# Performance work log

Measured on AMD Instinct MI355X. Metric: run time of the kernel, lower is better.

Reference implementation:

```python
import jax, jax.numpy as jnp
import numpy as np

B, H, D, HD = 16384, 8, 256, 128  # batch, heads, dim, hidden_dim


def setup_inputs() -> dict:
    key = jax.random.key(0)
    ks = jax.random.split(key, 8)
    return {
        "x": jax.random.normal(ks[0], (B, D), dtype=jnp.float32),
        "h": jax.random.normal(ks[1], (B, H, HD), dtype=jnp.float32),
        "sigmoid_w": jax.random.normal(ks[2], (H, HD + D, 2), dtype=jnp.float32),
        "sigmoid_b": jax.random.normal(ks[3], (H, 2), dtype=jnp.float32),
        "tanh_w": jax.random.normal(ks[4], (H, HD + D, HD), dtype=jnp.float32),
        "tanh_b": jax.random.normal(ks[5], (H, HD), dtype=jnp.float32),
        "out_w": jax.random.normal(ks[6], (H, HD, D), dtype=jnp.float32),
        "out_b": jax.random.normal(ks[7], (H, D), dtype=jnp.float32),
    }


def reference(x, h, sigmoid_w, sigmoid_b, tanh_w, tanh_b, out_w, out_b):
    # x: [B, D] -> broadcast across heads: [B, H, D]
    x_ = jnp.broadcast_to(x[:, None, :], (x.shape[0], h.shape[1], x.shape[1]))
    # gate input: [B, H, hidden+dim]
    sig_in = jnp.concatenate([h, x_], axis=2)
    sigmoids = jax.nn.sigmoid(jnp.einsum('bhm,hmn->bhn', sig_in, sigmoid_w) + sigmoid_b)
    # reset-gated hidden concat with x: [B, H, hidden+dim]
    tanh_in = jnp.concatenate([sigmoids[:, :, :1] * h, x_], axis=2)
    cand = jnp.tanh(jnp.einsum('bhm,hmn->bhn', tanh_in, tanh_w) + tanh_b)
    proportion = sigmoids[:, :, 1:]
    new_h = (1 - proportion) * h + proportion * cand
    output = jnp.einsum('bhm,hmn->bhn', new_h, out_w) + out_b
    return (output, new_h)
```

## Files before the change

### kernel.cpp

```cpp
#include <hip/hip_runtime.h>
#include <math.h>

typedef short bf16x8 __attribute__((ext_vector_type(8)));
typedef short bf16x4 __attribute__((ext_vector_type(4)));
typedef float floatx4 __attribute__((ext_vector_type(4)));
typedef float floatx2 __attribute__((ext_vector_type(2)));
typedef float floatx16 __attribute__((ext_vector_type(16)));

#define NB   16384
#define H8   8
#define ND   256
#define NHD  128
#define NK   384

__device__ __forceinline__ unsigned short f2bf(float f) {
  unsigned int u = __float_as_uint(f);
  u += 0x7FFFu + ((u >> 16) & 1u);
  return (unsigned short)(u >> 16);
}
__device__ __forceinline__ float bf2f(unsigned short s) {
  return __uint_as_float(((unsigned int)s) << 16);
}
__device__ __forceinline__ float fast_sigmoid(float z) {
  z = fminf(fmaxf(z, -60.f), 60.f);
  return __builtin_amdgcn_rcpf(1.f + __expf(-z));
}
__device__ __forceinline__ float fast_tanh(float s) {
  s = fminf(fmaxf(s, -9.f), 9.f);
  float e = __expf(2.f * s);
  return (e - 1.f) * __builtin_amdgcn_rcpf(e + 1.f);
}

#define WTP (H8 * 24 * 4 * 512)
#define WOP (H8 * 8 * 8 * 512)
#define XFP (NB * ND)
#define NGATE (NB * H8)
#define WS_NEED3 ((size_t)(WTP + WOP + XFP) * 2 + (size_t)2 * NGATE * 4)

__global__ void prep3c(const float* __restrict__ tanh_w,
                       const float* __restrict__ sig_w,
                       const float* __restrict__ sig_b,
                       const float* __restrict__ out_w,
                       const float* __restrict__ x,
                       const float* __restrict__ h,
                       short* __restrict__ wtp_hi,
                       short* __restrict__ wop,
                       short* __restrict__ xfh,
                       float* __restrict__ gW, float* __restrict__ pW) {
  __shared__ float smem[14480];
  const int t = threadIdx.x;
  const int b = blockIdx.x;
  if (b < 192) {
    float* tile = smem;
    int head = b / 24, ks = b % 24;
    const float* slab = tanh_w + ((size_t)head * NK + ks * 16) * NHD;
#pragma unroll
    for (int it = 0; it < 2; ++it) {
      int i = it * 256 + t;
      floatx4 v = reinterpret_cast<const floatx4*>(slab)[i];
      int r = i >> 5, c4 = i & 31;
      *reinterpret_cast<floatx4*>(&tile[r * 132 + c4 * 4]) = v;
    }
    __syncthreads();
    int ct = t >> 6, l = t & 63;
    bf16x8 hi8;
#pragma unroll
    for (int j = 0; j < 8; ++j) {
      float w = tile[((l >> 5) * 8 + j) * 132 + ct * 32 + (l & 31)];
      hi8[j] = (short)f2bf(w);
    }
    size_t dst = ((((size_t)head * 24 + ks) * 4 + ct) * 64 + l) * 8;
    *reinterpret_cast<bf16x8*>(wtp_hi + dst) = hi8;
  } else if (b < 256) {
    float* tile = smem;
    int head = (b - 192) / 8, ks = (b - 192) % 8;
    const float* slab = out_w + ((size_t)head * NHD + ks * 16) * ND;
#pragma unroll
    for (int it = 0; it < 4; ++it) {
      int i = it * 256 + t;
      floatx4 v = reinterpret_cast<const floatx4*>(slab)[i];
      int r = i >> 6, c4 = i & 63;
      *reinterpret_cast<floatx4*>(&tile[r * 260 + c4 * 4]) = v;
    }
    __syncthreads();
#pragma unroll
    for (int u = 0; u < 2; ++u) {
      int idx = u * 256 + t;
      int ct = idx >> 6, l = idx & 63;
      bf16x8 o8;
#pragma unroll
      for (int j = 0; j < 8; ++j) {
        float w = tile[((l >> 5) * 8 + j) * 260 + ct * 32 + (l & 31)];
        o8[j] = (short)f2bf(w);
      }
      size_t dst = ((((size_t)head * 8 + ks) * 8 + ct) * 64 + l) * 8;
      *reinterpret_cast<bf16x8*>(wop + dst) = o8;
    }
  } else if (b < 2304) {
    int i = (b - 256) * 256 + t;
    int bb = i >> 5, c0 = (i & 31) * 8;
    const float* xp = x + (size_t)bb * ND + c0;
    floatx4 v0 = *reinterpret_cast<const floatx4*>(xp);
    floatx4 v1 = *reinterpret_cast<const floatx4*>(xp + 4);
    bf16x8 h8;
#pragma unroll
    for (int j = 0; j < 4; ++j) {
      h8[j] = (short)f2bf(v0[j]);
      h8[4 + j] = (short)f2bf(v1[j]);
    }
    int dst = ((bb >> 5) * 16 + (c0 >> 4)) * 512 +
              (((c0 >> 3) & 1) * 32 + (bb & 31)) * 8;
    *reinterpret_cast<bf16x8*>(xfh + dst) = h8;
  } else {
    float* xs = smem;
    float* ws = smem + 8320;
    int gb = b - 2304;
    long rowb = (long)gb * 32;
#pragma unroll
    for (int it = 0; it < 8; ++it) {
      int idx = it * 256 + t;
      int r = idx >> 6, c4 = idx & 63;
      floatx4 v = *reinterpret_cast<const floatx4*>(x + (rowb + r) * ND + c4 * 4);
      *reinterpret_cast<floatx4*>(&xs[r * 260 + c4 * 4]) = v;
    }
#pragma unroll
    for (int it = 0; it < 12; ++it) {
      int idx = it * 256 + t;
      floatx2 v = *reinterpret_cast<const floatx2*>(sig_w + (size_t)idx * 2);
      int head = idx / 384;
      int rem = idx * 2 - head * 768;
      *reinterpret_cast<floatx2*>(&ws[head * 770 + rem]) = v;
    }
    __syncthreads();
    int bl = t >> 3, head = t & 7;
    const float* hrow = h + (rowb * 8 + t) * 128;
    const float* wh = &ws[head * 770];
    float a0 = 0.f, a1 = 0.f;
#pragma unroll 8
    for (int k4 = 0; k4 < 32; ++k4) {
      floatx4 hv = *reinterpret_cast<const floatx4*>(hrow + k4 * 4);
#pragma unroll
      for (int j = 0; j < 4; ++j) {
        floatx2 w2 = *reinterpret_cast<const floatx2*>(&wh[(k4 * 4 + j) * 2]);
        a0 += hv[j] * w2[0];
        a1 += hv[j] * w2[1];
      }
    }
    const float* xrow = &xs[bl * 260];
#pragma unroll 8
    for (int k4 = 0; k4 < 64; ++k4) {
      floatx4 xv = *reinterpret_cast<const floatx4*>(xrow + k4 * 4);
#pragma unroll
      for (int j = 0; j < 4; ++j) {
        floatx2 w2 = *reinterpret_cast<const floatx2*>(&wh[(128 + k4 * 4 + j) * 2]);
        a0 += xv[j] * w2[0];
        a1 += xv[j] * w2[1];
      }
    }
    long gi = rowb * 8 + t;
    gW[gi] = fast_sigmoid(a0 + sig_b[head * 2 + 0]);
    pW[gi] = fast_sigmoid(a1 + sig_b[head * 2 + 1]);
  }
}

__global__ __launch_bounds__(256, 4) void gru3(
    const float* __restrict__ h,
    const float* __restrict__ tanh_b, const float* __restrict__ out_b,
    const short* __restrict__ wtp_hi, const short* __restrict__ wop,
    const short* __restrict__ xfh,
    const float* __restrict__ gW, const float* __restrict__ pW,
    float* __restrict__ out, float* __restrict__ out_nh) {
  __shared__ __align__(16) short AhH[16 * 512];
  __shared__ __align__(16) short AhL[16 * 512];
  __shared__ float pbuf[64];

  const int t = threadIdx.x;
  const int lane = t & 63;
  const int cq = t >> 6;
  const int l31 = lane & 31;
  const int lh = lane >> 5;
  const int head = (int)(blockIdx.x >> 8);
  const int rb = (int)(blockIdx.x & 255);
  const long rowbase = (long)rb * 64;

  if (t < 64) pbuf[t] = pW[(rowbase + t) * H8 + head];

#pragma unroll
  for (int it = 0; it < 4; ++it) {
    int gi = it * 256 + t;
    int row = gi >> 4, kc = gi & 15;
    float g = gW[(rowbase + row) * H8 + head];
    const float* hp = h + ((rowbase + row) * H8 + head) * NHD + kc * 8;
    floatx4 v0 = *reinterpret_cast<const floatx4*>(hp);
    floatx4 v1 = *reinterpret_cast<const floatx4*>(hp + 4);
    bf16x8 hi8, lo8;
#pragma unroll
    for (int j = 0; j < 4; ++j) {
      float s0 = g * v0[j];
      unsigned short hb = f2bf(s0);
      hi8[j] = (short)hb; lo8[j] = (short)f2bf(s0 - bf2f(hb));
      float s1 = g * v1[j];
      unsigned short hb2 = f2bf(s1);
      hi8[4 + j] = (short)hb2; lo8[4 + j] = (short)f2bf(s1 - bf2f(hb2));
    }
    int rg = row >> 5, row32 = row & 31;
    int chunk = (rg * 8 + (kc >> 1)) * 64 + (kc & 1) * 32 + row32;
    *reinterpret_cast<bf16x8*>(&AhH[chunk * 8]) = hi8;
    *reinterpret_cast<bf16x8*>(&AhL[chunk * 8]) = lo8;
  }
  __syncthreads();

  const short* __restrict__ xh0 = xfh + ((size_t)(rb * 2 + 0) * 16 * 512) + lane * 8;
  const short* __restrict__ xh1 = xfh + ((size_t)(rb * 2 + 1) * 16 * 512) + lane * 8;
  const short* __restrict__ bh_p = wtp_hi + (((size_t)head * 24 * 4 + cq) * 512) + lane * 8;

  floatx16 acc0, acc1;
#pragma unroll
  for (int z = 0; z < 16; ++z) { acc0[z] = 0.f; acc1[z] = 0.f; }

  bf16x8 bhA = *reinterpret_cast<const bf16x8*>(bh_p);
  bf16x8 bhB = *reinterpret_cast<const bf16x8*>(bh_p + 2048);
#pragma unroll
  for (int ks = 0; ks < 8; ++ks) {
    bf16x8 bh = bhA; bhA = bhB;
    bhB = *reinterpret_cast<const bf16x8*>(bh_p + (ks + 2) * 2048);
    bf16x8 a0h = *reinterpret_cast<const bf16x8*>(&AhH[(ks * 64 + lane) * 8]);
    bf16x8 a0l = *reinterpret_cast<const bf16x8*>(&AhL[(ks * 64 + lane) * 8]);
    bf16x8 a1h = *reinterpret_cast<const bf16x8*>(&AhH[((8 + ks) * 64 + lane) * 8]);
    bf16x8 a1l = *reinterpret_cast<const bf16x8*>(&AhL[((8 + ks) * 64 + lane) * 8]);
    acc0 = __builtin_amdgcn_mfma_f32_32x32x16_bf16(a0h, bh, acc0, 0, 0, 0);
    acc0 = __builtin_amdgcn_mfma_f32_32x32x16_bf16(a0l, bh, acc0, 0, 0, 0);
    acc1 = __builtin_amdgcn_mfma_f32_32x32x16_bf16(a1h, bh, acc1, 0, 0, 0);
    acc1 = __builtin_amdgcn_mfma_f32_32x32x16_bf16(a1l, bh, acc1, 0, 0, 0);
  }
  {
    bf16x8 x0A = *reinterpret_cast<const bf16x8*>(xh0);
    bf16x8 x1A = *reinterpret_cast<const bf16x8*>(xh1);
    bf16x8 x0B = *reinterpret_cast<const bf16x8*>(xh0 + 512);
    bf16x8 x1B = *reinterpret_cast<const bf16x8*>(xh1 + 512);
#pragma unroll
    for (int xk = 0; xk < 16; ++xk) {
      const int ks = 8 + xk;
      bf16x8 bh = bhA; bhA = bhB;
      if (ks + 2 < 24) bhB = *reinterpret_cast<const bf16x8*>(bh_p + (ks + 2) * 2048);
      bf16x8 x0 = x0A, x1 = x1A;
      x0A = x0B; x1A = x1B;
      if (xk + 2 < 16) {
        x0B = *reinterpret_cast<const bf16x8*>(xh0 + (xk + 2) * 512);
        x1B = *reinterpret_cast<const bf16x8*>(xh1 + (xk + 2) * 512);
      }
      acc0 = __builtin_amdgcn_mfma_f32_32x32x16_bf16(x0, bh, acc0, 0, 0, 0);
      acc1 = __builtin_amdgcn_mfma_f32_32x32x16_bf16(x1, bh, acc1, 0, 0, 0);
    }
  }
  __syncthreads();

  const int col = cq * 32 + l31;
  const float tb = tanh_b[head * NHD + col];
  const float* __restrict__ hcol = h + (rowbase * H8 + head) * NHD + col;
#define EPI(RG, ACC)                                                          \
  {                                                                           \
    _Pragma("unroll")                                                         \
    for (int reg = 0; reg < 16; ++reg) {                                      \
      int crow = (reg & 3) + 8 * (reg >> 2) + 4 * lh;                         \
      int row = RG * 32 + crow;                                               \
      float p = pbuf[row];                                                    \
      float cand = fast_tanh(ACC[reg] + tb);                                  \
      float hv = hcol[(size_t)row * (H8 * NHD)];                              \
      float nh = hv + p * (cand - hv);                                        \
      int el = ((RG * 8 + (col >> 4)) * 64 + ((l31 >> 3) & 1) * 32 + crow) * 8 + (col & 7); \
      out_nh[((rowbase + row) * H8 + head) * NHD + col] = nh;                 \
      AhH[el] = (short)f2bf(nh);                                              \
    }                                                                         \
  }
  EPI(0, acc0)
  EPI(1, acc1)
#undef EPI
  __syncthreads();

  const short* __restrict__ wo_p = wop + (((size_t)head * 64 + cq * 2) * 512) + lane * 8;
  const float ob0 = out_b[head * ND + cq * 64 + l31];
  const float ob1 = out_b[head * ND + cq * 64 + 32 + l31];
#define OUTP(RG)                                                              \
  {                                                                           \
    floatx16 a3a, a3b;                                                        \
    _Pragma("unroll")                                                         \
    for (int z = 0; z < 16; ++z) { a3a[z] = 0.f; a3b[z] = 0.f; }              \
    bf16x8 w0n = *reinterpret_cast<const bf16x8*>(wo_p);                      \
    bf16x8 w1n = *reinterpret_cast<const bf16x8*>(wo_p + 512);                \
    _Pragma("unroll")                                                         \
    for (int ks = 0; ks < 8; ++ks) {                                          \
      bf16x8 w0 = w0n, w1 = w1n;                                              \
      if (ks < 7) {                                                           \
        w0n = *reinterpret_cast<const bf16x8*>(wo_p + (ks + 1) * 4096);       \
        w1n = *reinterpret_cast<const bf16x8*>(wo_p + (ks + 1) * 4096 + 512); \
      }                                                                       \
      bf16x8 a = *reinterpret_cast<const bf16x8*>(&AhH[((RG * 8 + ks) * 64 + lane) * 8]); \
      a3a = __builtin_amdgcn_mfma_f32_32x32x16_bf16(a, w0, a3a, 0, 0, 0);     \
      a3b = __builtin_amdgcn_mfma_f32_32x32x16_bf16(a, w1, a3b, 0, 0, 0);     \
    }                                                                         \
    _Pragma("unroll")                                                         \
    for (int reg = 0; reg < 16; ++reg) {                                      \
      int row = RG * 32 + (reg & 3) + 8 * (reg >> 2) + 4 * lh;                \
      long obase = ((rowbase + row) * H8 + head) * ND;                        \
      out[obase + cq * 64 + l31] = a3a[reg] + ob0;                            \
      out[obase + cq * 64 + 32 + l31] = a3b[reg] + ob1;                       \
    }                                                                         \
  }
  OUTP(0)
  OUTP(1)
#undef OUTP
}

#define WT_ELEMS (H8 * NK * NHD)
#define WO_ELEMS (H8 * NHD * ND)

__global__ void prep_kernel(const float* __restrict__ tanh_w,
                            const float* __restrict__ out_w,
                            short* __restrict__ wt_hi,
                            short* __restrict__ wt_lo,
                            short* __restrict__ wo) {
  const int total1 = WT_ELEMS;
  const int total2 = WO_ELEMS;
  for (int i = blockIdx.x * blockDim.x + threadIdx.x; i < total1 + total2;
       i += gridDim.x * blockDim.x) {
    if (i < total1) {
      int hh = i / (NK * NHD);
      int rem = i - hh * NK * NHD;
      int k = rem / NHD, n = rem - k * NHD;
      float w = tanh_w[i];
      unsigned short hi = f2bf(w);
      unsigned short lo = f2bf(w - bf2f(hi));
      int dst = hh * (48 * NHD * 8) + (k >> 3) * (NHD * 8) + n * 8 + (k & 7);
      wt_hi[dst] = (short)hi;
      wt_lo[dst] = (short)lo;
    } else {
      int j = i - total1;
      int hh = j / (NHD * ND);
      int rem = j - hh * NHD * ND;
      int k = rem / ND, n = rem - k * ND;
      int dst = hh * (16 * ND * 8) + (k >> 3) * (ND * 8) + n * 8 + (k & 7);
      wo[dst] = (short)f2bf(out_w[j]);
    }
  }
}

#define BM   32
#define NT   512
#define LDA 392
#define LDNH 136

__global__ __launch_bounds__(NT, 4) void gru_main(
    const float* __restrict__ x, const float* __restrict__ h,
    const float* __restrict__ sig_w, const float* __restrict__ sig_b,
    const float* __restrict__ tanh_b, const float* __restrict__ out_b,
    const short* __restrict__ wt_hi, const short* __restrict__ wt_lo,
    const short* __restrict__ wo,
    float* __restrict__ out, float* __restrict__ out_nh) {
  __shared__ __align__(16) short Ahi[BM][LDA];
  __shared__ __align__(16) short Alo[BM][LDA];
  __shared__ __align__(16) short NHL[BM][LDNH];
  __shared__ floatx2 swl[NK];
  __shared__ float gbuf[BM], pbuf[BM];

  const int t = threadIdx.x;
  const int lane = t & 63;
  const int wid = t >> 6;
  const int wrow = wid >> 2;
  const int wcol = wid & 3;
  const int ln = lane & 15;
  const int kg = lane >> 4;
  const int head = blockIdx.x & 7;
  const long rowbase = (long)(blockIdx.x >> 3) * BM;
  const int arow = wrow * 16 + ln;

#pragma unroll
  for (int i = 0; i < 4; ++i) {
    int idx = i * NT + t;
    int r = idx >> 6, c4 = idx & 63;
    floatx4 v = *reinterpret_cast<const floatx4*>(x + (rowbase + r) * ND + c4 * 4);
    bf16x4 hi, lo;
#pragma unroll
    for (int j = 0; j < 4; ++j) {
      unsigned short hb = f2bf(v[j]);
      hi[j] = (short)hb;
      lo[j] = (short)f2bf(v[j] - bf2f(hb));
    }
    *reinterpret_cast<bf16x4*>(&Ahi[r][NHD + c4 * 4]) = hi;
    *reinterpret_cast<bf16x4*>(&Alo[r][NHD + c4 * 4]) = lo;
  }
#pragma unroll
  for (int i = 0; i < 2; ++i) {
    int idx = i * NT + t;
    int r = idx >> 5, c4 = idx & 31;
    floatx4 v = *reinterpret_cast<const floatx4*>(
        h + ((rowbase + r) * H8 + head) * NHD + c4 * 4);
    bf16x4 hi, lo;
#pragma unroll
    for (int j = 0; j < 4; ++j) {
      unsigned short hb = f2bf(v[j]);
      hi[j] = (short)hb;
      lo[j] = (short)f2bf(v[j] - bf2f(hb));
    }
    *reinterpret_cast<bf16x4*>(&Ahi[r][c4 * 4]) = hi;
    *reinterpret_cast<bf16x4*>(&Alo[r][c4 * 4]) = lo;
  }
  if (t < NK)
    swl[t] = *reinterpret_cast<const floatx2*>(sig_w + ((size_t)head * NK + t) * 2);
  __syncthreads();
  {
    int r = t >> 4, u = t & 15;
    float a0 = 0.f, a1 = 0.f;
#pragma unroll
    for (int kk = 0; kk < 24; ++kk) {
      int k = u + kk * 16;
      float a = bf2f((unsigned short)Ahi[r][k]) + bf2f((unsigned short)Alo[r][k]);
      floatx2 w = swl[k];
      a0 += a * w[0];
      a1 += a * w[1];
    }
#pragma unroll
    for (int off = 1; off < 16; off <<= 1) {
      a0 += __shfl_xor(a0, off);
      a1 += __shfl_xor(a1, off);
    }
    if (u == 0) {
      gbuf[r] = fast_sigmoid(a0 + sig_b[head * 2 + 0]);
      pbuf[r] = fast_sigmoid(a1 + sig_b[head * 2 + 1]);
    }
  }
  floatx4 acc1[2] = {{0.f, 0.f, 0.f, 0.f}, {0.f, 0.f, 0.f, 0.f}};
  floatx4 acc2[2] = {{0.f, 0.f, 0.f, 0.f}, {0.f, 0.f, 0.f, 0.f}};
  const size_t wtbase = (size_t)head * (48 * NHD * 8);
#pragma unroll
  for (int ks = 0; ks < 12; ++ks) {
    bf16x8 ahi = *reinterpret_cast<const bf16x8*>(&Ahi[arow][ks * 32 + kg * 8]);
    bf16x8 alo = *reinterpret_cast<const bf16x8*>(&Alo[arow][ks * 32 + kg * 8]);
    floatx4* acc = (ks < 4) ? acc1 : acc2;
#pragma unroll
    for (int cf = 0; cf < 2; ++cf) {
      int n0 = wcol * 32 + cf * 16;
      size_t woff = wtbase + (size_t)(ks * 4 + kg) * (NHD * 8) + (size_t)(n0 + ln) * 8;
      bf16x8 bhi = *reinterpret_cast<const bf16x8*>(wt_hi + woff);
      bf16x8 blo = *reinterpret_cast<const bf16x8*>(wt_lo + woff);
      acc[cf] = __builtin_amdgcn_mfma_f32_16x16x32_bf16(ahi, bhi, acc[cf], 0, 0, 0);
      acc[cf] = __builtin_amdgcn_mfma_f32_16x16x32_bf16(alo, bhi, acc[cf], 0, 0, 0);
      acc[cf] = __builtin_amdgcn_mfma_f32_16x16x32_bf16(ahi, blo, acc[cf], 0, 0, 0);
    }
  }
  __syncthreads();
#pragma unroll
  for (int cf = 0; cf < 2; ++cf) {
    int col = wcol * 32 + cf * 16 + ln;
    float tb = tanh_b[head * NHD + col];
#pragma unroll
    for (int j = 0; j < 4; ++j) {
      int r = wrow * 16 + kg * 4 + j;
      float g = gbuf[r], p = pbuf[r];
      float s = g * acc1[cf][j] + acc2[cf][j] + tb;
      float cand = fast_tanh(s);
      float hv = bf2f((unsigned short)Ahi[r][col]) + bf2f((unsigned short)Alo[r][col]);
      float nh = hv + p * (cand - hv);
      out_nh[((rowbase + r) * H8 + head) * NHD + col] = nh;
      NHL[r][col] = (short)f2bf(nh);
    }
  }
  __syncthreads();
  floatx4 acc3[4] = {{0.f, 0.f, 0.f, 0.f}, {0.f, 0.f, 0.f, 0.f},
                     {0.f, 0.f, 0.f, 0.f}, {0.f, 0.f, 0.f, 0.f}};
  const size_t wobase = (size_t)head * (16 * ND * 8);
#pragma unroll
  for (int ks = 0; ks < 4; ++ks) {
    bf16x8 a = *reinterpret_cast<const bf16x8*>(&NHL[arow][ks * 32 + kg * 8]);
#pragma unroll
    for (int cf = 0; cf < 4; ++cf) {
      int n0 = wcol * 64 + cf * 16;
      size_t woff = wobase + (size_t)(ks * 4 + kg) * (ND * 8) + (size_t)(n0 + ln) * 8;
      bf16x8 bfr = *reinterpret_cast<const bf16x8*>(wo + woff);
      acc3[cf] = __builtin_amdgcn_mfma_f32_16x16x32_bf16(a, bfr, acc3[cf], 0, 0, 0);
    }
  }
#pragma unroll
  for (int cf = 0; cf < 4; ++cf) {
    int col = wcol * 64 + cf * 16 + ln;
    float ob = out_b[head * ND + col];
#pragma unroll
    for (int j = 0; j < 4; ++j) {
      int r = wrow * 16 + kg * 4 + j;
      out[((rowbase + r) * H8 + head) * ND + col] = acc3[cf][j] + ob;
    }
  }
}

extern "C" void kernel_launch(void* const* d_in, const int* in_sizes, int n_in,
                              void* d_out, int out_size, void* d_ws, size_t ws_size,
                              hipStream_t stream) {
  (void)in_sizes; (void)n_in; (void)out_size;
  const float* x      = (const float*)d_in[0];
  const float* h      = (const float*)d_in[1];
  const float* sig_w  = (const float*)d_in[2];
  const float* sig_b  = (const float*)d_in[3];
  const float* tanh_w = (const float*)d_in[4];
  const float* tanh_b = (const float*)d_in[5];
  const float* out_w  = (const float*)d_in[6];
  const float* out_b  = (const float*)d_in[7];

  float* out = (float*)d_out;
  float* out_nh = out + (size_t)NB * H8 * ND;

  if (ws_size >= WS_NEED3) {
    short* wtp_hi = (short*)d_ws;
    short* wop    = wtp_hi + WTP;
    short* xfh    = wop + WOP;
    float* gW     = (float*)(xfh + XFP);
    float* pW     = gW + NGATE;
    hipLaunchKernelGGL(prep3c, dim3(256 + 2048 + 512), dim3(256), 0, stream,
                       tanh_w, sig_w, sig_b, out_w, x, h,
                       wtp_hi, wop, xfh, gW, pW);
    hipLaunchKernelGGL(gru3, dim3((NB / 64) * H8), dim3(256), 0, stream,
                       h, tanh_b, out_b, wtp_hi, wop, xfh, gW, pW,
                       out, out_nh);
  } else {
    short* wt_hi = (short*)d_ws;
    short* wt_lo = wt_hi + WT_ELEMS;
    short* wo    = wt_lo + WT_ELEMS;
    hipLaunchKernelGGL(prep_kernel, dim3(512), dim3(256), 0, stream,
                       tanh_w, out_w, wt_hi, wt_lo, wo);
    hipLaunchKernelGGL(gru_main, dim3((NB / BM) * H8), dim3(NT), 0, stream,
                       x, h, sig_w, sig_b, tanh_b, out_b, wt_hi, wt_lo, wo,
                       out, out_nh);
  }
}
```

Measured before the change: 92.12 us.

## Fuse sigmoid gate computation into main GRU kernel and swizzle LDS layout

Moves the sigmoid gate dot products out of the prep kernel into the main kernel: each block computes its 64 rows' gates with four lanes per row and a shuffle reduction, so the gate arrays no longer make a round trip through global memory. The h loads are issued before the gate computation and held in registers. It also applies an XOR swizzle to the shared-memory A-operand layout to reduce bank conflicts. The cost is that h and x are re-read for the gate math (eight times for x, once per head) and register pressure rises.

```diff
diff --git a/kernel.cpp b/kernel.cpp
--- a/kernel.cpp
+++ b/kernel.cpp
@@ -30,28 +30,25 @@
   float e = __expf(2.f * s);
   return (e - 1.f) * __builtin_amdgcn_rcpf(e + 1.f);
 }
+__device__ __forceinline__ int swz(int idx16) {
+  return idx16 ^ ((idx16 >> 6) & 7);
+}
 
 #define WTP (H8 * 24 * 4 * 512)
 #define WOP (H8 * 8 * 8 * 512)
 #define XFP (NB * ND)
-#define NGATE (NB * H8)
-#define WS_NEED3 ((size_t)(WTP + WOP + XFP) * 2 + (size_t)2 * NGATE * 4)
+#define WS_NEED3 ((size_t)(WTP + WOP + XFP) * 2)
 
 __global__ void prep3c(const float* __restrict__ tanh_w,
-                       const float* __restrict__ sig_w,
-                       const float* __restrict__ sig_b,
                        const float* __restrict__ out_w,
                        const float* __restrict__ x,
-                       const float* __restrict__ h,
                        short* __restrict__ wtp_hi,
                        short* __restrict__ wop,
-                       short* __restrict__ xfh,
-                       float* __restrict__ gW, float* __restrict__ pW) {
-  __shared__ float smem[14480];
+                       short* __restrict__ xfh) {
+  __shared__ float tile[16 * 260];
   const int t = threadIdx.x;
   const int b = blockIdx.x;
   if (b < 192) {
-    float* tile = smem;
     int head = b / 24, ks = b % 24;
     const float* slab = tanh_w + ((size_t)head * NK + ks * 16) * NHD;
 #pragma unroll
@@ -72,7 +69,6 @@
     size_t dst = ((((size_t)head * 24 + ks) * 4 + ct) * 64 + l) * 8;
     *reinterpret_cast<bf16x8*>(wtp_hi + dst) = hi8;
   } else if (b < 256) {
-    float* tile = smem;
     int head = (b - 192) / 8, ks = (b - 192) % 8;
     const float* slab = out_w + ((size_t)head * NHD + ks * 16) * ND;
 #pragma unroll
@@ -96,7 +92,7 @@
       size_t dst = ((((size_t)head * 8 + ks) * 8 + ct) * 64 + l) * 8;
       *reinterpret_cast<bf16x8*>(wop + dst) = o8;
     }
-  } else if (b < 2304) {
+  } else {
     int i = (b - 256) * 256 + t;
     int bb = i >> 5, c0 = (i & 31) * 8;
     const float* xp = x + (size_t)bb * ND + c0;
@@ -111,68 +107,19 @@
     int dst = ((bb >> 5) * 16 + (c0 >> 4)) * 512 +
               (((c0 >> 3) & 1) * 32 + (bb & 31)) * 8;
     *reinterpret_cast<bf16x8*>(xfh + dst) = h8;
-  } else {
-    float* xs = smem;
-    float* ws = smem + 8320;
-    int gb = b - 2304;
-    long rowb = (long)gb * 32;
-#pragma unroll
-    for (int it = 0; it < 8; ++it) {
-      int idx = it * 256 + t;
-      int r = idx >> 6, c4 = idx & 63;
-      floatx4 v = *reinterpret_cast<const floatx4*>(x + (rowb + r) * ND + c4 * 4);
-      *reinterpret_cast<floatx4*>(&xs[r * 260 + c4 * 4]) = v;
-    }
-#pragma unroll
-    for (int it = 0; it < 12; ++it) {
-      int idx = it * 256 + t;
-      floatx2 v = *reinterpret_cast<const floatx2*>(sig_w + (size_t)idx * 2);
-      int head = idx / 384;
-      int rem = idx * 2 - head * 768;
-      *reinterpret_cast<floatx2*>(&ws[head * 770 + rem]) = v;
-    }
-    __syncthreads();
-    int bl = t >> 3, head = t & 7;
-    const float* hrow = h + (rowb * 8 + t) * 128;
-    const float* wh = &ws[head * 770];
-    float a0 = 0.f, a1 = 0.f;
-#pragma unroll 8
-    for (int k4 = 0; k4 < 32; ++k4) {
-      floatx4 hv = *reinterpret_cast<const floatx4*>(hrow + k4 * 4);
-#pragma unroll
-      for (int j = 0; j < 4; ++j) {
-        floatx2 w2 = *reinterpret_cast<const floatx2*>(&wh[(k4 * 4 + j) * 2]);
-        a0 += hv[j] * w2[0];
-        a1 += hv[j] * w2[1];
-      }
-    }
-    const float* xrow = &xs[bl * 260];
-#pragma unroll 8
-    for (int k4 = 0; k4 < 64; ++k4) {
-      floatx4 xv = *reinterpret_cast<const floatx4*>(xrow + k4 * 4);
-#pragma unroll
-      for (int j = 0; j < 4; ++j) {
-        floatx2 w2 = *reinterpret_cast<const floatx2*>(&wh[(128 + k4 * 4 + j) * 2]);
-        a0 += xv[j] * w2[0];
-        a1 += xv[j] * w2[1];
-      }
-    }
-    long gi = rowb * 8 + t;
-    gW[gi] = fast_sigmoid(a0 + sig_b[head * 2 + 0]);
-    pW[gi] = fast_sigmoid(a1 + sig_b[head * 2 + 1]);
   }
 }
 
 __global__ __launch_bounds__(256, 4) void gru3(
-    const float* __restrict__ h,
+    const float* __restrict__ h, const float* __restrict__ x,
+    const float* __restrict__ sig_w, const float* __restrict__ sig_b,
     const float* __restrict__ tanh_b, const float* __restrict__ out_b,
     const short* __restrict__ wtp_hi, const short* __restrict__ wop,
     const short* __restrict__ xfh,
-    const float* __restrict__ gW, const float* __restrict__ pW,
     float* __restrict__ out, float* __restrict__ out_nh) {
   __shared__ __align__(16) short AhH[16 * 512];
   __shared__ __align__(16) short AhL[16 * 512];
-  __shared__ float pbuf[64];
+  __shared__ float gbuf[64], pbuf[64];
 
   const int t = threadIdx.x;
   const int lane = t & 63;
@@ -183,30 +130,63 @@
   const int rb = (int)(blockIdx.x & 255);
   const long rowbase = (long)rb * 64;
 
-  if (t < 64) pbuf[t] = pW[(rowbase + t) * H8 + head];
-
+  floatx4 hreg[4][2];
+  int srow[4], skc[4];
 #pragma unroll
   for (int it = 0; it < 4; ++it) {
     int gi = it * 256 + t;
     int row = gi >> 4, kc = gi & 15;
-    float g = gW[(rowbase + row) * H8 + head];
+    srow[it] = row; skc[it] = kc;
     const float* hp = h + ((rowbase + row) * H8 + head) * NHD + kc * 8;
-    floatx4 v0 = *reinterpret_cast<const floatx4*>(hp);
-    floatx4 v1 = *reinterpret_cast<const floatx4*>(hp + 4);
+    hreg[it][0] = *reinterpret_cast<const floatx4*>(hp);
+    hreg[it][1] = *reinterpret_cast<const floatx4*>(hp + 4);
+  }
+
+  {
+    int r = t >> 2, u = t & 3;
+    const float* hrow = h + ((rowbase + r) * H8 + head) * NHD;
+    const float* xrow = x + (rowbase + r) * ND;
+    const float* wsp = sig_w + (size_t)head * NK * 2;
+    float a0 = 0.f, a1 = 0.f;
+#pragma unroll
+    for (int i = 0; i < 24; ++i) {
+      int k = u * 96 + i * 4;
+      floatx4 av = (k < 128)
+          ? *reinterpret_cast<const floatx4*>(hrow + k)
+          : *reinterpret_cast<const floatx4*>(xrow + (k - 128));
+      floatx4 w01 = *reinterpret_cast<const floatx4*>(wsp + k * 2);
+      floatx4 w23 = *reinterpret_cast<const floatx4*>(wsp + k * 2 + 4);
+      a0 += av[0] * w01[0] + av[1] * w01[2] + av[2] * w23[0] + av[3] * w23[2];
+      a1 += av[0] * w01[1] + av[1] * w01[3] + av[2] * w23[1] + av[3] * w23[3];
+    }
+    a0 += __shfl_xor(a0, 1); a0 += __shfl_xor(a0, 2);
+    a1 += __shfl_xor(a1, 1); a1 += __shfl_xor(a1, 2);
+    if (u == 0) {
+      gbuf[r] = fast_sigmoid(a0 + sig_b[head * 2 + 0]);
+      pbuf[r] = fast_sigmoid(a1 + sig_b[head * 2 + 1]);
+    }
+  }
+  __syncthreads();
+
+#pragma unroll
+  for (int it = 0; it < 4; ++it) {
+    int row = srow[it], kc = skc[it];
+    float g = gbuf[row];
     bf16x8 hi8, lo8;
 #pragma unroll
     for (int j = 0; j < 4; ++j) {
-      float s0 = g * v0[j];
+      float s0 = g * hreg[it][0][j];
       unsigned short hb = f2bf(s0);
       hi8[j] = (short)hb; lo8[j] = (short)f2bf(s0 - bf2f(hb));
-      float s1 = g * v1[j];
+      float s1 = g * hreg[it][1][j];
       unsigned short hb2 = f2bf(s1);
       hi8[4 + j] = (short)hb2; lo8[4 + j] = (short)f2bf(s1 - bf2f(hb2));
     }
     int rg = row >> 5, row32 = row & 31;
     int chunk = (rg * 8 + (kc >> 1)) * 64 + (kc & 1) * 32 + row32;
-    *reinterpret_cast<bf16x8*>(&AhH[chunk * 8]) = hi8;
-    *reinterpret_cast<bf16x8*>(&AhL[chunk * 8]) = lo8;
+    int sc = swz(chunk);
+    *reinterpret_cast<bf16x8*>(&AhH[sc * 8]) = hi8;
+    *reinterpret_cast<bf16x8*>(&AhL[sc * 8]) = lo8;
   }
   __syncthreads();
 
@@ -224,10 +204,10 @@
   for (int ks = 0; ks < 8; ++ks) {
     bf16x8 bh = bhA; bhA = bhB;
     bhB = *reinterpret_cast<const bf16x8*>(bh_p + (ks + 2) * 2048);
-    bf16x8 a0h = *reinterpret_cast<const bf16x8*>(&AhH[(ks * 64 + lane) * 8]);
-    bf16x8 a0l = *reinterpret_cast<const bf16x8*>(&AhL[(ks * 64 + lane) * 8]);
-    bf16x8 a1h = *reinterpret_cast<const bf16x8*>(&AhH[((8 + ks) * 64 + lane) * 8]);
-    bf16x8 a1l = *reinterpret_cast<const bf16x8*>(&AhL[((8 + ks) * 64 + lane) * 8]);
+    bf16x8 a0h = *reinterpret_cast<const bf16x8*>(&AhH[swz(ks * 64 + lane) * 8]);
+    bf16x8 a0l = *reinterpret_cast<const bf16x8*>(&AhL[swz(ks * 64 + lane) * 8]);
+    bf16x8 a1h = *reinterpret_cast<const bf16x8*>(&AhH[swz((8 + ks) * 64 + lane) * 8]);
+    bf16x8 a1l = *reinterpret_cast<const bf16x8*>(&AhL[swz((8 + ks) * 64 + lane) * 8]);
     acc0 = __builtin_amdgcn_mfma_f32_32x32x16_bf16(a0h, bh, acc0, 0, 0, 0);
     acc0 = __builtin_amdgcn_mfma_f32_32x32x16_bf16(a0l, bh, acc0, 0, 0, 0);
     acc1 = __builtin_amdgcn_mfma_f32_32x32x16_bf16(a1h, bh, acc1, 0, 0, 0);
@@ -268,9 +248,9 @@
       float cand = fast_tanh(ACC[reg] + tb);                                  \
       float hv = hcol[(size_t)row * (H8 * NHD)];                              \
       float nh = hv + p * (cand - hv);                                        \
-      int el = ((RG * 8 + (col >> 4)) * 64 + ((l31 >> 3) & 1) * 32 + crow) * 8 + (col & 7); \
+      int el16 = (RG * 8 + (col >> 4)) * 64 + ((l31 >> 3) & 1) * 32 + crow;   \
       out_nh[((rowbase + row) * H8 + head) * NHD + col] = nh;                 \
-      AhH[el] = (short)f2bf(nh);                                              \
+      AhH[swz(el16) * 8 + (col & 7)] = (short)f2bf(nh);                       \
     }                                                                         \
   }
   EPI(0, acc0)
@@ -295,7 +275,7 @@
         w0n = *reinterpret_cast<const bf16x8*>(wo_p + (ks + 1) * 4096);       \
         w1n = *reinterpret_cast<const bf16x8*>(wo_p + (ks + 1) * 4096 + 512); \
       }                                                                       \
-      bf16x8 a = *reinterpret_cast<const bf16x8*>(&AhH[((RG * 8 + ks) * 64 + lane) * 8]); \
+      bf16x8 a = *reinterpret_cast<const bf16x8*>(&AhH[swz((RG * 8 + ks) * 64 + lane) * 8]); \
       a3a = __builtin_amdgcn_mfma_f32_32x32x16_bf16(a, w0, a3a, 0, 0, 0);     \
       a3b = __builtin_amdgcn_mfma_f32_32x32x16_bf16(a, w1, a3b, 0, 0, 0);     \
     }                                                                         \
@@ -512,13 +492,10 @@
     short* wtp_hi = (short*)d_ws;
     short* wop    = wtp_hi + WTP;
     short* xfh    = wop + WOP;
-    float* gW     = (float*)(xfh + XFP);
-    float* pW     = gW + NGATE;
-    hipLaunchKernelGGL(prep3c, dim3(256 + 2048 + 512), dim3(256), 0, stream,
-                       tanh_w, sig_w, sig_b, out_w, x, h,
-                       wtp_hi, wop, xfh, gW, pW);
+    hipLaunchKernelGGL(prep3c, dim3(256 + 2048), dim3(256), 0, stream,
+                       tanh_w, out_w, x, wtp_hi, wop, xfh);
     hipLaunchKernelGGL(gru3, dim3((NB / 64) * H8), dim3(256), 0, stream,
-                       h, tanh_b, out_b, wtp_hi, wop, xfh, gW, pW,
+                       h, x, sig_w, sig_b, tanh_b, out_b, wtp_hi, wop, xfh,
                        out, out_nh);
   } else {
     short* wt_hi = (short*)d_ws;
```

After: 139.1 us. +51.0%, slower.
